# Kernel optimization log

Measured on AMD Instinct MI355X. Metric: run time of the kernel, lower is better.

The kernel has to match this reference:

```python
import jax, jax.numpy as jnp
import numpy as np
from jax import lax

SLOPE = 8.0  # sigmoid_slope
N = 2048
C = 2
B = 256
T = 256


def setup_inputs() -> dict:
    key = jax.random.key(0)
    ks = jax.random.split(key, 6)
    std = 1.0 / np.sqrt(N)
    inputs = jax.random.normal(ks[0], (C, B, T), dtype=jnp.float32)
    state0 = jnp.zeros((B, N), dtype=jnp.float32)
    mask = jnp.ones((N,), dtype=jnp.float32)
    encoders = std * jax.random.normal(ks[1], (C, N), dtype=jnp.float32)
    decoders = std * jax.random.normal(ks[2], (C, N), dtype=jnp.float32)
    # W ~ N(0, 1/n): spectral radius ~1; rescale to init_radius=0.97
    W = 0.97 * std * jax.random.normal(ks[3], (N, N), dtype=jnp.float32)
    bias = jnp.zeros((N,), dtype=jnp.float32)
    thresholds = 0.5 * jnp.ones((N,), dtype=jnp.float32)  # sigmoid_threshold
    return {"inputs": inputs, "state0": state0, "mask": mask,
            "encoders": encoders, "decoders": decoders, "W": W,
            "bias": bias, "thresholds": thresholds}


def reference(inputs, state0, mask, encoders, decoders, W, bias, thresholds):
    # inputs: [C, B, T]; state0: [B, N]; mask/bias/thresholds: [N]
    def step(state, x_t):  # x_t: [C, B]
        ext = jnp.einsum('cb,cn->bn', x_t, encoders)           # external current
        pre = (state + mask * ext) @ W.T                       # [B, N]
        new_state = mask * (bias + jax.nn.sigmoid(SLOPE * (pre - thresholds)))
        outs = jnp.einsum('bn,cn->cb', new_state, decoders)    # [C, B]
        return new_state, outs

    xs = jnp.transpose(inputs, (2, 0, 1))                      # [T, C, B]
    _, outs = lax.scan(step, state0, xs)                       # [T, C, B]
    return jnp.transpose(outs, (1, 2, 0))                      # [C, B, T]
```

## Files before the change

kernel.cpp:

```cpp
#include <hip/hip_runtime.h>


#define NN 2048
#define BB 256
#define TT 256
#define SLOPE 8.0f

#define NBLK 256
#define NTH  512
#define NSB  8

#define MRGS 68
#define RSZW (32*MRGS)
#define LDS_R0    0
#define LDS_CONST (4*RSZW*4)
#define LDS_TOTAL (LDS_CONST + 7*64*4)

#define WS_FLAGS 0
#define WS_SBUF  32768
#define SBUF_SZ  131072
#define WS_PART  (32768 + 8*NSB*SBUF_SZ)

typedef short s16x8 __attribute__((ext_vector_type(8)));
typedef float f32x16 __attribute__((ext_vector_type(16)));
typedef unsigned u32x4 __attribute__((ext_vector_type(4)));
typedef unsigned u32x2 __attribute__((ext_vector_type(2)));

__device__ __forceinline__ unsigned f2bf1(float f) {
  union { float f; unsigned u; } v; v.f = f;
  return (v.u + 0x7fffu + ((v.u >> 16) & 1u)) >> 16;
}
__device__ __forceinline__ unsigned pack2(float a, float b) {
  return f2bf1(a) | (f2bf1(b) << 16);
}

__device__ __forceinline__ void store_b64_sys(void* p, u32x2 v) {
  asm volatile("global_store_dwordx2 %0, %1, off sc0 sc1" :: "v"(p), "v"(v) : "memory");
}
__device__ __forceinline__ void store_u32_sys(void* p, unsigned v) {
  asm volatile("global_store_dword %0, %1, off sc0 sc1" :: "v"(p), "v"(v) : "memory");
}

#define LOAD_A(dst, base, OFF) \
  asm volatile("global_load_dwordx4 %0, %1, off offset:" #OFF \
               : "=v"(dst) : "v"(base) : "memory")

__device__ __forceinline__ void grid_barrier(unsigned* flags, int gbase, int member,
                                             unsigned tval, bool do_inv) {
  asm volatile("s_waitcnt vmcnt(0)" ::: "memory");
  __syncthreads();
  const int tid = threadIdx.x;
  if (tid == 0)
    __hip_atomic_store(&flags[(gbase + member) * 32], tval,
                       __ATOMIC_RELAXED, __HIP_MEMORY_SCOPE_SYSTEM);
  if (tid < 64) {
    for (;;) {
      unsigned v = __hip_atomic_load(&flags[(gbase + (tid & 31)) * 32],
                                     __ATOMIC_RELAXED, __HIP_MEMORY_SCOPE_SYSTEM);
      if (__all(v >= tval)) break;
      __builtin_amdgcn_s_sleep(1);
    }
  }
  __syncthreads();
  if (do_inv) {
    if (tid < 64) __builtin_amdgcn_fence(__ATOMIC_ACQUIRE, "agent");
    __syncthreads();
  }
}

__global__ __launch_bounds__(NTH, 2)
void mc_integrator_kernel(const float* __restrict__ x, const float* __restrict__ state0,
                          const float* __restrict__ mask, const float* __restrict__ enc,
                          const float* __restrict__ dec, const float* __restrict__ W,
                          const float* __restrict__ bias, const float* __restrict__ thr,
                          char* __restrict__ ws)
{
  extern __shared__ char lds[];
  const int tid = threadIdx.x;
  const int blk = blockIdx.x;
  const int g   = blk & 7;
  const int bnx = blk >> 3;
  const int C0  = bnx * 64;
  const int kq  = tid >> 6;
  const int lane = tid & 63;

  unsigned* flags = (unsigned*)(ws + WS_FLAGS);
  char* sbufs = ws + WS_SBUF;
  unsigned* partials = (unsigned*)(ws + WS_PART);

  float* cmask = (float*)(lds + LDS_CONST);
  float* cbias = cmask + 64; float* cthr  = cbias + 64;
  float* cenc0 = cthr  + 64; float* cenc1 = cenc0 + 64;
  float* cdec0 = cenc1 + 64; float* cdec1 = cdec0 + 64;
  if (tid < 64) {
    int n = C0 + tid;
    cmask[tid] = mask[n]; cbias[tid] = bias[n]; cthr[tid] = thr[n];
    cenc0[tid] = enc[n];  cenc1[tid] = enc[NN + n];
    cdec0[tid] = dec[n];  cdec1[tid] = dec[NN + n];
  }

  s16x8 Breg[32];
  {
    const float* wb = W + (size_t)(C0 + (lane & 31)) * NN
                        + kq*256 + (lane >> 5)*8;
    #pragma unroll
    for (int c = 0; c < 32; ++c) {
      const float* p = wb + (size_t)((c & 1)*32)*NN + (c >> 1)*16;
      float4 lo = *(const float4*)p;
      float4 hi = *(const float4*)(p + 4);
      union { u32x4 u; s16x8 s; } cv;
      cv.u = (u32x4){ pack2(lo.x, lo.y), pack2(lo.z, lo.w),
                      pack2(hi.x, hi.y), pack2(hi.z, hi.w) };
      Breg[c] = cv.s;
    }
  }

  __syncthreads();

  const int r_row = tid >> 4, cg = tid & 15;
  const int bg = g * 32 + r_row;
  const unsigned s_off = (unsigned)((bnx*4 + (cg>>2))*1024
                                    + ((((cg>>1)&1) << 5) + r_row)*16 + (cg&1)*8);

  {
    const float* s0p = state0 + (size_t)bg*NN + C0 + cg*4;
    float4 s4 = *(const float4*)s0p;
    float x0 = x[(size_t)bg*TT];
    float x1 = x[(size_t)(BB*TT) + (size_t)bg*TT];
    float sv[4] = {s4.x, s4.y, s4.z, s4.w};
    #pragma unroll
    for (int j = 0; j < 4; ++j) {
      int nl = cg*4 + j;
      sv[j] += cmask[nl] * (x0*cenc0[nl] + x1*cenc1[nl]);
    }
    u32x2 pk = { pack2(sv[0], sv[1]), pack2(sv[2], sv[3]) };
    store_b64_sys(sbufs + (size_t)g*NSB*SBUF_SZ + s_off, pk);
  }
  grid_barrier(flags, g*32, bnx, 1u, true);

  const int colc = lane & 31, rowb = 4 * (lane >> 5);
  float* mreg = (float*)(lds + LDS_R0) + (kq >> 1) * RSZW;
  unsigned pdpk = 0;

  for (int t = 0; t < TT; ++t) {
    const char* sb = sbufs + (size_t)(g*NSB + (t & (NSB-1))) * SBUF_SZ;
    char*       sn = sbufs + (size_t)(g*NSB + ((t+1) & (NSB-1))) * SBUF_SZ;

    if (t > 0 && cg == 0)
      store_u32_sys(&partials[((size_t)(t-1)*32 + bnx)*256 + bg], pdpk);
    float x0n = 0.f, x1n = 0.f;
    if (t < TT - 1) {
      x0n = x[(size_t)bg*TT + t + 1];
      x1n = x[(size_t)(BB*TT) + (size_t)bg*TT + t + 1];
    }

    if (t & (NSB-1)) {
      if (lane < 4) {
        const unsigned tvc = (unsigned)(t + 1);
        for (;;) {
          unsigned v = __hip_atomic_load(&flags[(g*32 + kq*4 + lane) * 32],
                                         __ATOMIC_RELAXED, __HIP_MEMORY_SCOPE_SYSTEM);
          if (__all(v >= tvc)) break;
          __builtin_amdgcn_s_sleep(1);
        }
      }
    }

    const char* ap = sb + (unsigned)(kq*16*1024) + (unsigned)(lane*16);
    s16x8 Ar[8];
    {
      const char* b0 = ap;
      LOAD_A(Ar[0], b0, 0);    LOAD_A(Ar[1], b0, 1024);
      LOAD_A(Ar[2], b0, 2048); LOAD_A(Ar[3], b0, 3072);
      const char* b1 = ap + 4096;
      LOAD_A(Ar[4], b1, 0);    LOAD_A(Ar[5], b1, 1024);
      LOAD_A(Ar[6], b1, 2048); LOAD_A(Ar[7], b1, 3072);
    }

    f32x16 acc0 = {0,0,0,0,0,0,0,0,0,0,0,0,0,0,0,0};
    f32x16 acc1 = {0,0,0,0,0,0,0,0,0,0,0,0,0,0,0,0};

    asm volatile("s_waitcnt vmcnt(4)"
      : "+v"(Ar[0]),"+v"(Ar[1]),"+v"(Ar[2]),"+v"(Ar[3]));
    #pragma unroll
    for (int i = 0; i < 4; ++i) {
      acc0 = __builtin_amdgcn_mfma_f32_32x32x16_bf16(Ar[i], Breg[i*2+0], acc0, 0,0,0);
      acc1 = __builtin_amdgcn_mfma_f32_32x32x16_bf16(Ar[i], Breg[i*2+1], acc1, 0,0,0);
    }
    {
      const char* b2 = ap + 8192;
      LOAD_A(Ar[0], b2, 0);    LOAD_A(Ar[1], b2, 1024);
      LOAD_A(Ar[2], b2, 2048); LOAD_A(Ar[3], b2, 3072);
    }
    asm volatile("s_waitcnt vmcnt(4)"
      : "+v"(Ar[4]),"+v"(Ar[5]),"+v"(Ar[6]),"+v"(Ar[7]));
    #pragma unroll
    for (int i = 0; i < 4; ++i) {
      acc0 = __builtin_amdgcn_mfma_f32_32x32x16_bf16(Ar[4+i], Breg[(4+i)*2+0], acc0, 0,0,0);
      acc1 = __builtin_amdgcn_mfma_f32_32x32x16_bf16(Ar[4+i], Breg[(4+i)*2+1], acc1, 0,0,0);
    }
    {
      const char* b3 = ap + 12288;
      LOAD_A(Ar[4], b3, 0);    LOAD_A(Ar[5], b3, 1024);
      LOAD_A(Ar[6], b3, 2048); LOAD_A(Ar[7], b3, 3072);
    }
    asm volatile("s_waitcnt vmcnt(4)"
      : "+v"(Ar[0]),"+v"(Ar[1]),"+v"(Ar[2]),"+v"(Ar[3]));
    #pragma unroll
    for (int i = 0; i < 4; ++i) {
      acc0 = __builtin_amdgcn_mfma_f32_32x32x16_bf16(Ar[i], Breg[(8+i)*2+0], acc0, 0,0,0);
      acc1 = __builtin_amdgcn_mfma_f32_32x32x16_bf16(Ar[i], Breg[(8+i)*2+1], acc1, 0,0,0);
    }
    asm volatile("s_waitcnt vmcnt(0)"
      : "+v"(Ar[4]),"+v"(Ar[5]),"+v"(Ar[6]),"+v"(Ar[7]));
    #pragma unroll
    for (int i = 0; i < 4; ++i) {
      acc0 = __builtin_amdgcn_mfma_f32_32x32x16_bf16(Ar[4+i], Breg[(12+i)*2+0], acc0, 0,0,0);
      acc1 = __builtin_amdgcn_mfma_f32_32x32x16_bf16(Ar[4+i], Breg[(12+i)*2+1], acc1, 0,0,0);
    }

    if (kq & 1) {
      #pragma unroll
      for (int r = 0; r < 16; ++r) {
        int row = rowb + (r & 3) + 8*(r >> 2);
        mreg[row*MRGS + colc]      = acc0[r];
        mreg[row*MRGS + 32 + colc] = acc1[r];
      }
    }
    __syncthreads();
    if (!(kq & 1)) {
      #pragma unroll
      for (int r = 0; r < 16; ++r) {
        int row = rowb + (r & 3) + 8*(r >> 2);
        mreg[row*MRGS + colc]      += acc0[r];
        mreg[row*MRGS + 32 + colc] += acc1[r];
      }
    }
    __syncthreads();

    {
      const float* m0 = (const float*)(lds + LDS_R0) + r_row*MRGS + cg*4;
      float4 q0 = *(const float4*)(m0);
      float4 q1 = *(const float4*)(m0 + RSZW);
      float4 q2 = *(const float4*)(m0 + 2*RSZW);
      float4 q3 = *(const float4*)(m0 + 3*RSZW);
      float pr[4] = {q0.x+q1.x+q2.x+q3.x, q0.y+q1.y+q2.y+q3.y,
                     q0.z+q1.z+q2.z+q3.z, q0.w+q1.w+q2.w+q3.w};
      float st[4];
      #pragma unroll
      for (int j = 0; j < 4; ++j) {
        int nl = cg*4 + j;
        float sg = 1.0f / (1.0f + __expf(-SLOPE * (pr[j] - cthr[nl])));
        st[j] = cmask[nl] * (cbias[nl] + sg);
      }
      if (t < TT - 1) {
        float sv[4];
        #pragma unroll
        for (int j = 0; j < 4; ++j) {
          int nl = cg*4 + j;
          sv[j] = st[j] + cmask[nl] * (x0n*cenc0[nl] + x1n*cenc1[nl]);
        }
        u32x2 pk = { pack2(sv[0], sv[1]), pack2(sv[2], sv[3]) };
        store_b64_sys(sn + s_off, pk);
      }
      float d0 = 0.f, d1 = 0.f;
      #pragma unroll
      for (int j = 0; j < 4; ++j) {
        int nl = cg*4 + j;
        d0 += st[j] * cdec0[nl];
        d1 += st[j] * cdec1[nl];
      }
      d0 += __shfl_xor(d0, 1); d0 += __shfl_xor(d0, 2);
      d0 += __shfl_xor(d0, 4); d0 += __shfl_xor(d0, 8);
      d1 += __shfl_xor(d1, 1); d1 += __shfl_xor(d1, 2);
      d1 += __shfl_xor(d1, 4); d1 += __shfl_xor(d1, 8);
      pdpk = pack2(d0, d1);
    }

    if (t < TT - 1) {
      if (((t + 1) & (NSB-1)) == 0) {
        grid_barrier(flags, g*32, bnx, (unsigned)(t + 2), true);
      } else {
        asm volatile("s_waitcnt vmcnt(0)" ::: "memory");
        __syncthreads();
        if (tid == 0)
          __hip_atomic_store(&flags[(g*32 + bnx) * 32], (unsigned)(t + 2),
                             __ATOMIC_RELAXED, __HIP_MEMORY_SCOPE_SYSTEM);
      }
    }
  }
  if (cg == 0)
    store_u32_sys(&partials[((size_t)(TT-1)*32 + bnx)*256 + bg], pdpk);
}

__global__ __launch_bounds__(256)
void reduce_out_kernel(const unsigned* __restrict__ partials, float* __restrict__ out) {
  const int t = blockIdx.x;
  const int b = threadIdx.x;
  const unsigned* p = partials + (size_t)t * 32 * 256 + b;
  float s0 = 0.f, s1 = 0.f;
  #pragma unroll
  for (int bn = 0; bn < 32; ++bn) {
    unsigned v = p[bn * 256];
    union { unsigned u; float f; } lo, hi;
    lo.u = v << 16; hi.u = v & 0xffff0000u;
    s0 += lo.f; s1 += hi.f;
  }
  out[(size_t)b * TT + t] = s0;
  out[(size_t)(BB * TT) + (size_t)b * TT + t] = s1;
}

extern "C" void kernel_launch(void* const* d_in, const int* in_sizes, int n_in,
                              void* d_out, int out_size, void* d_ws, size_t ws_size,
                              hipStream_t stream) {
  const float* x      = (const float*)d_in[0];
  const float* state0 = (const float*)d_in[1];
  const float* mask   = (const float*)d_in[2];
  const float* enc    = (const float*)d_in[3];
  const float* dec    = (const float*)d_in[4];
  const float* W      = (const float*)d_in[5];
  const float* bias   = (const float*)d_in[6];
  const float* thr    = (const float*)d_in[7];
  float* out = (float*)d_out;
  char*  ws  = (char*)d_ws;

  (void)hipMemsetAsync(ws, 0, 32768, stream);

  (void)hipFuncSetAttribute((const void*)mc_integrator_kernel,
                            hipFuncAttributeMaxDynamicSharedMemorySize, LDS_TOTAL);

  void* args[] = { (void*)&x, (void*)&state0, (void*)&mask, (void*)&enc, (void*)&dec,
                   (void*)&W, (void*)&bias, (void*)&thr, (void*)&ws };
  (void)hipLaunchCooperativeKernel((const void*)mc_integrator_kernel,
                                   dim3(NBLK), dim3(NTH), args, (unsigned)LDS_TOTAL, stream);

  const unsigned* partials = (const unsigned*)(ws + WS_PART);
  reduce_out_kernel<<<dim3(TT), dim3(256), 0, stream>>>(partials, out);
}
```

Before: 1.255 ms.

## Detect XCC co-location at runtime and use L2-coherent fast path without periodic grid barriers

Each block records its hardware XCC ID. If all 32 blocks of a batch group share one XCC and the groups sit on distinct XCCs, a templated fast time loop runs. It uses plain stores and sc0 loads that stay coherent through the shared L2, avoids system-scope writes, and replaces the periodic full grid barrier plus acquire fence with per-step flag polling. Otherwise the original system-scope path runs. This cuts cross-die coherence traffic and barrier overhead, but it depends on the hardware scheduler's block-to-XCC placement, and the runtime check adds a startup barrier.

Result: no change. 1.243 ms (-1.0%).

```diff
diff --git a/kernel.cpp b/kernel.cpp
--- a/kernel.cpp
+++ b/kernel.cpp
@@ -14,12 +14,14 @@
 #define RSZW (32*MRGS)
 #define LDS_R0    0
 #define LDS_CONST (4*RSZW*4)
-#define LDS_TOTAL (LDS_CONST + 7*64*4)
+#define LDS_MISC  (LDS_CONST + 7*64*4)
+#define LDS_TOTAL (LDS_MISC + 16)
 
 #define WS_FLAGS 0
-#define WS_SBUF  32768
+#define WS_XCC   32768
+#define WS_SBUF  65536
 #define SBUF_SZ  131072
-#define WS_PART  (32768 + 8*NSB*SBUF_SZ)
+#define WS_PART  (65536 + 8*NSB*SBUF_SZ)
 
 typedef short s16x8 __attribute__((ext_vector_type(8)));
 typedef float f32x16 __attribute__((ext_vector_type(16)));
@@ -41,9 +43,13 @@
   asm volatile("global_store_dword %0, %1, off sc0 sc1" :: "v"(p), "v"(v) : "memory");
 }
 
-#define LOAD_A(dst, base, OFF) \
-  asm volatile("global_load_dwordx4 %0, %1, off offset:" #OFF \
-               : "=v"(dst) : "v"(base) : "memory")
+template<bool FAST>
+__device__ __forceinline__ void load_a16(s16x8& d, const char* a) {
+  if constexpr (FAST)
+    asm volatile("global_load_dwordx4 %0, %1, off sc0" : "=v"(d) : "v"(a) : "memory");
+  else
+    asm volatile("global_load_dwordx4 %0, %1, off"     : "=v"(d) : "v"(a) : "memory");
+}
 
 __device__ __forceinline__ void grid_barrier(unsigned* flags, int gbase, int member,
                                              unsigned tval, bool do_inv) {
@@ -68,78 +74,25 @@
   }
 }
 
-__global__ __launch_bounds__(NTH, 2)
-void mc_integrator_kernel(const float* __restrict__ x, const float* __restrict__ state0,
-                          const float* __restrict__ mask, const float* __restrict__ enc,
-                          const float* __restrict__ dec, const float* __restrict__ W,
-                          const float* __restrict__ bias, const float* __restrict__ thr,
-                          char* __restrict__ ws)
+template<bool FAST>
+__device__ __forceinline__ void time_loop(const float* __restrict__ x,
+    unsigned* flags, char* sbufs, unsigned* partials, char* lds,
+    const s16x8 (&Breg)[32], int g, int bnx)
 {
-  extern __shared__ char lds[];
-  const int tid = threadIdx.x;
-  const int blk = blockIdx.x;
-  const int g   = blk & 7;
-  const int bnx = blk >> 3;
-  const int C0  = bnx * 64;
-  const int kq  = tid >> 6;
+  const int tid  = threadIdx.x;
+  const int kq   = tid >> 6;
   const int lane = tid & 63;
-
-  unsigned* flags = (unsigned*)(ws + WS_FLAGS);
-  char* sbufs = ws + WS_SBUF;
-  unsigned* partials = (unsigned*)(ws + WS_PART);
-
-  float* cmask = (float*)(lds + LDS_CONST);
-  float* cbias = cmask + 64; float* cthr  = cbias + 64;
-  float* cenc0 = cthr  + 64; float* cenc1 = cenc0 + 64;
-  float* cdec0 = cenc1 + 64; float* cdec1 = cdec0 + 64;
-  if (tid < 64) {
-    int n = C0 + tid;
-    cmask[tid] = mask[n]; cbias[tid] = bias[n]; cthr[tid] = thr[n];
-    cenc0[tid] = enc[n];  cenc1[tid] = enc[NN + n];
-    cdec0[tid] = dec[n];  cdec1[tid] = dec[NN + n];
-  }
-
-  s16x8 Breg[32];
-  {
-    const float* wb = W + (size_t)(C0 + (lane & 31)) * NN
-                        + kq*256 + (lane >> 5)*8;
-    #pragma unroll
-    for (int c = 0; c < 32; ++c) {
-      const float* p = wb + (size_t)((c & 1)*32)*NN + (c >> 1)*16;
-      float4 lo = *(const float4*)p;
-      float4 hi = *(const float4*)(p + 4);
-      union { u32x4 u; s16x8 s; } cv;
-      cv.u = (u32x4){ pack2(lo.x, lo.y), pack2(lo.z, lo.w),
-                      pack2(hi.x, hi.y), pack2(hi.z, hi.w) };
-      Breg[c] = cv.s;
-    }
-  }
-
-  __syncthreads();
-
+  const int colc = lane & 31, rowb = 4 * (lane >> 5);
   const int r_row = tid >> 4, cg = tid & 15;
   const int bg = g * 32 + r_row;
   const unsigned s_off = (unsigned)((bnx*4 + (cg>>2))*1024
                                     + ((((cg>>1)&1) << 5) + r_row)*16 + (cg&1)*8);
-
-  {
-    const float* s0p = state0 + (size_t)bg*NN + C0 + cg*4;
-    float4 s4 = *(const float4*)s0p;
-    float x0 = x[(size_t)bg*TT];
-    float x1 = x[(size_t)(BB*TT) + (size_t)bg*TT];
-    float sv[4] = {s4.x, s4.y, s4.z, s4.w};
-    #pragma unroll
-    for (int j = 0; j < 4; ++j) {
-      int nl = cg*4 + j;
-      sv[j] += cmask[nl] * (x0*cenc0[nl] + x1*cenc1[nl]);
-    }
-    u32x2 pk = { pack2(sv[0], sv[1]), pack2(sv[2], sv[3]) };
-    store_b64_sys(sbufs + (size_t)g*NSB*SBUF_SZ + s_off, pk);
-  }
-  grid_barrier(flags, g*32, bnx, 1u, true);
-
-  const int colc = lane & 31, rowb = 4 * (lane >> 5);
   float* mreg = (float*)(lds + LDS_R0) + (kq >> 1) * RSZW;
+  const float* cmask = (const float*)(lds + LDS_CONST);
+  const float* cbias = cmask + 64; const float* cthr  = cbias + 64;
+  const float* cenc0 = cthr  + 64; const float* cenc1 = cenc0 + 64;
+  const float* cdec0 = cenc1 + 64; const float* cdec1 = cdec0 + 64;
+
   unsigned pdpk = 0;
 
   for (int t = 0; t < TT; ++t) {
@@ -154,9 +107,10 @@
       x1n = x[(size_t)(BB*TT) + (size_t)bg*TT + t + 1];
     }
 
-    if (t & (NSB-1)) {
+    const bool need_poll = FAST ? (t > 0) : ((t & (NSB-1)) != 0);
+    if (need_poll) {
       if (lane < 4) {
-        const unsigned tvc = (unsigned)(t + 1);
+        const unsigned tvc = (unsigned)(t + 2);
         for (;;) {
           unsigned v = __hip_atomic_load(&flags[(g*32 + kq*4 + lane) * 32],
                                          __ATOMIC_RELAXED, __HIP_MEMORY_SCOPE_SYSTEM);
@@ -168,14 +122,8 @@
 
     const char* ap = sb + (unsigned)(kq*16*1024) + (unsigned)(lane*16);
     s16x8 Ar[8];
-    {
-      const char* b0 = ap;
-      LOAD_A(Ar[0], b0, 0);    LOAD_A(Ar[1], b0, 1024);
-      LOAD_A(Ar[2], b0, 2048); LOAD_A(Ar[3], b0, 3072);
-      const char* b1 = ap + 4096;
-      LOAD_A(Ar[4], b1, 0);    LOAD_A(Ar[5], b1, 1024);
-      LOAD_A(Ar[6], b1, 2048); LOAD_A(Ar[7], b1, 3072);
-    }
+    #pragma unroll
+    for (int i = 0; i < 8; ++i) load_a16<FAST>(Ar[i], ap + i*1024);
 
     f32x16 acc0 = {0,0,0,0,0,0,0,0,0,0,0,0,0,0,0,0};
     f32x16 acc1 = {0,0,0,0,0,0,0,0,0,0,0,0,0,0,0,0};
@@ -187,11 +135,9 @@
       acc0 = __builtin_amdgcn_mfma_f32_32x32x16_bf16(Ar[i], Breg[i*2+0], acc0, 0,0,0);
       acc1 = __builtin_amdgcn_mfma_f32_32x32x16_bf16(Ar[i], Breg[i*2+1], acc1, 0,0,0);
     }
-    {
-      const char* b2 = ap + 8192;
-      LOAD_A(Ar[0], b2, 0);    LOAD_A(Ar[1], b2, 1024);
-      LOAD_A(Ar[2], b2, 2048); LOAD_A(Ar[3], b2, 3072);
-    }
+    #pragma unroll
+    for (int i = 0; i < 4; ++i) load_a16<FAST>(Ar[i], ap + (8+i)*1024);
+
     asm volatile("s_waitcnt vmcnt(4)"
       : "+v"(Ar[4]),"+v"(Ar[5]),"+v"(Ar[6]),"+v"(Ar[7]));
     #pragma unroll
@@ -199,11 +145,9 @@
       acc0 = __builtin_amdgcn_mfma_f32_32x32x16_bf16(Ar[4+i], Breg[(4+i)*2+0], acc0, 0,0,0);
       acc1 = __builtin_amdgcn_mfma_f32_32x32x16_bf16(Ar[4+i], Breg[(4+i)*2+1], acc1, 0,0,0);
     }
-    {
-      const char* b3 = ap + 12288;
-      LOAD_A(Ar[4], b3, 0);    LOAD_A(Ar[5], b3, 1024);
-      LOAD_A(Ar[6], b3, 2048); LOAD_A(Ar[7], b3, 3072);
-    }
+    #pragma unroll
+    for (int i = 0; i < 4; ++i) load_a16<FAST>(Ar[4+i], ap + (12+i)*1024);
+
     asm volatile("s_waitcnt vmcnt(4)"
       : "+v"(Ar[0]),"+v"(Ar[1]),"+v"(Ar[2]),"+v"(Ar[3]));
     #pragma unroll
@@ -261,7 +205,8 @@
           sv[j] = st[j] + cmask[nl] * (x0n*cenc0[nl] + x1n*cenc1[nl]);
         }
         u32x2 pk = { pack2(sv[0], sv[1]), pack2(sv[2], sv[3]) };
-        store_b64_sys(sn + s_off, pk);
+        if constexpr (FAST) *(u32x2*)(sn + s_off) = pk;
+        else                store_b64_sys(sn + s_off, pk);
       }
       float d0 = 0.f, d1 = 0.f;
       #pragma unroll
@@ -278,19 +223,115 @@
     }
 
     if (t < TT - 1) {
-      if (((t + 1) & (NSB-1)) == 0) {
-        grid_barrier(flags, g*32, bnx, (unsigned)(t + 2), true);
+      if (!FAST && ((t + 1) & (NSB-1)) == 0) {
+        grid_barrier(flags, g*32, bnx, (unsigned)(t + 3), true);
       } else {
         asm volatile("s_waitcnt vmcnt(0)" ::: "memory");
         __syncthreads();
         if (tid == 0)
-          __hip_atomic_store(&flags[(g*32 + bnx) * 32], (unsigned)(t + 2),
+          __hip_atomic_store(&flags[(g*32 + bnx) * 32], (unsigned)(t + 3),
                              __ATOMIC_RELAXED, __HIP_MEMORY_SCOPE_SYSTEM);
       }
     }
   }
   if (cg == 0)
     store_u32_sys(&partials[((size_t)(TT-1)*32 + bnx)*256 + bg], pdpk);
+}
+
+__global__ __launch_bounds__(NTH, 2)
+void mc_integrator_kernel(const float* __restrict__ x, const float* __restrict__ state0,
+                          const float* __restrict__ mask, const float* __restrict__ enc,
+                          const float* __restrict__ dec, const float* __restrict__ W,
+                          const float* __restrict__ bias, const float* __restrict__ thr,
+                          char* __restrict__ ws)
+{
+  extern __shared__ char lds[];
+  const int tid = threadIdx.x;
+  const int blk = blockIdx.x;
+  const int g   = blk & 7;
+  const int bnx = blk >> 3;
+  const int C0  = bnx * 64;
+  const int kq  = tid >> 6, lane = tid & 63;
+
+  unsigned* flags = (unsigned*)(ws + WS_FLAGS);
+  unsigned* xccs  = (unsigned*)(ws + WS_XCC);
+  char* sbufs = ws + WS_SBUF;
+  unsigned* partials = (unsigned*)(ws + WS_PART);
+
+  float* cmask = (float*)(lds + LDS_CONST);
+  float* cbias = cmask + 64; float* cthr  = cbias + 64;
+  float* cenc0 = cthr  + 64; float* cenc1 = cenc0 + 64;
+  float* cdec0 = cenc1 + 64; float* cdec1 = cdec0 + 64;
+  if (tid < 64) {
+    int n = C0 + tid;
+    cmask[tid] = mask[n]; cbias[tid] = bias[n]; cthr[tid] = thr[n];
+    cenc0[tid] = enc[n];  cenc1[tid] = enc[NN + n];
+    cdec0[tid] = dec[n];  cdec1[tid] = dec[NN + n];
+  }
+
+  s16x8 Breg[32];
+  {
+    const float* wb = W + (size_t)(C0 + (lane & 31)) * NN
+                        + kq*256 + (lane >> 5)*8;
+    #pragma unroll
+    for (int c = 0; c < 32; ++c) {
+      const float* p = wb + (size_t)((c & 1)*32)*NN + (c >> 1)*16;
+      float4 lo = *(const float4*)p;
+      float4 hi = *(const float4*)(p + 4);
+      union { u32x4 u; s16x8 s; } cv;
+      cv.u = (u32x4){ pack2(lo.x, lo.y), pack2(lo.z, lo.w),
+                      pack2(hi.x, hi.y), pack2(hi.z, hi.w) };
+      Breg[c] = cv.s;
+    }
+  }
+
+  unsigned myxcc;
+  asm volatile("s_getreg_b32 %0, hwreg(HW_REG_XCC_ID)" : "=s"(myxcc));
+  if (tid == 0) store_u32_sys(&xccs[g*32 + bnx], myxcc);
+
+  __syncthreads();
+  grid_barrier(flags, g*32, bnx, 1u, true);
+
+  if (tid < 32) {
+    int allco = 1, distinct = 0;
+    unsigned lead0 = 0;
+    #pragma unroll
+    for (int j = 0; j < 8; ++j) {
+      unsigned v = __hip_atomic_load(&xccs[j*32 + tid],
+                                     __ATOMIC_RELAXED, __HIP_MEMORY_SCOPE_SYSTEM);
+      unsigned u = (unsigned)__shfl((int)v, 0);
+      if (!__all(v == u)) allco = 0;
+      if (j == 0) lead0 = u; else if (u != lead0) distinct = 1;
+    }
+    if (tid == 0) *(volatile int*)(lds + LDS_MISC) = (allco && distinct) ? 1 : 0;
+  }
+  __syncthreads();
+  const bool fast = (*(volatile int*)(lds + LDS_MISC)) != 0;
+
+  {
+    const int r_row = tid >> 4, cg = tid & 15;
+    const int bg = g*32 + r_row;
+    const unsigned s_off = (unsigned)((bnx*4 + (cg>>2))*1024
+                                      + ((((cg>>1)&1) << 5) + r_row)*16 + (cg&1)*8);
+    const float* s0p = state0 + (size_t)bg*NN + C0 + cg*4;
+    float4 s4 = *(const float4*)s0p;
+    float x0 = x[(size_t)bg*TT];
+    float x1 = x[(size_t)(BB*TT) + (size_t)bg*TT];
+    float sv[4] = {s4.x, s4.y, s4.z, s4.w};
+    #pragma unroll
+    for (int j = 0; j < 4; ++j) {
+      int nl = cg*4 + j;
+      sv[j] += cmask[nl] * (x0*cenc0[nl] + x1*cenc1[nl]);
+    }
+    u32x2 pk = { pack2(sv[0], sv[1]), pack2(sv[2], sv[3]) };
+    char* dst = sbufs + (size_t)g*NSB*SBUF_SZ + s_off;
+    if (fast) *(u32x2*)dst = pk;
+    else      store_b64_sys(dst, pk);
+  }
+  grid_barrier(flags, g*32, bnx, 2u, !fast);
+
+  if (fast) time_loop<true >(x, flags, sbufs, partials, lds, Breg, g, bnx);
+  else      time_loop<false>(x, flags, sbufs, partials, lds, Breg, g, bnx);
 }
 
 __global__ __launch_bounds__(256)
```
